# Optimization experiments

Hardware: AMD Instinct MI355X
Metric: run time of the kernel (lower is better)

## Reference

```python
import jax, jax.numpy as jnp
import numpy as np

B, N, L = 2, 2048, 2048
DQ, DKV, H, WF = 1024, 1024, 16, 4
HD = DQ // H
EPS = 1e-5


def _ln(x, g, b):
    m = jnp.mean(x, axis=-1, keepdims=True)
    v = jnp.mean(jnp.square(x - m), axis=-1, keepdims=True)
    return (x - m) * jax.lax.rsqrt(v + EPS) * g + b


def setup_inputs() -> dict:
    key = jax.random.key(0)
    ks = jax.random.split(key, 12)
    s = 0.02
    return {
        "x_q": jax.random.normal(ks[0], (B, N, DQ), jnp.float32),
        "x_kv": jax.random.normal(ks[1], (B, L, DKV), jnp.float32),
        "qn_g": jnp.ones((DQ,), jnp.float32),
        "qn_b": jnp.zeros((DQ,), jnp.float32),
        "kvn_g": jnp.ones((DKV,), jnp.float32),
        "kvn_b": jnp.zeros((DKV,), jnp.float32),
        "Wq": jax.random.normal(ks[2], (DQ, DQ), jnp.float32) * s,
        "bq": jnp.zeros((DQ,), jnp.float32),
        "Wk": jax.random.normal(ks[3], (DQ, DKV), jnp.float32) * s,
        "bk": jnp.zeros((DQ,), jnp.float32),
        "Wv": jax.random.normal(ks[4], (DQ, DKV), jnp.float32) * s,
        "bv": jnp.zeros((DQ,), jnp.float32),
        "Wo": jax.random.normal(ks[5], (DQ, DQ), jnp.float32) * s,
        "bo": jnp.zeros((DQ,), jnp.float32),
        "n2_g": jnp.ones((DQ,), jnp.float32),
        "n2_b": jnp.zeros((DQ,), jnp.float32),
        "W1": jax.random.normal(ks[6], (WF * DQ, DQ), jnp.float32) * s,
        "b1": jnp.zeros((WF * DQ,), jnp.float32),
        "W2": jax.random.normal(ks[7], (DQ, WF * DQ), jnp.float32) * s,
        "b2": jnp.zeros((DQ,), jnp.float32),
    }


def reference(x_q, x_kv, qn_g, qn_b, kvn_g, kvn_b, Wq, bq, Wk, bk, Wv, bv,
              Wo, bo, n2_g, n2_b, W1, b1, W2, b2):
    # projections (torch Linear: x @ W.T + b)
    q = (_ln(x_q, qn_g, qn_b) @ Wq.T + bq).reshape(B, N, H, HD)
    kvn = _ln(x_kv, kvn_g, kvn_b)
    k = (kvn @ Wk.T + bk).reshape(B, L, H, HD)
    v = (kvn @ Wv.T + bv).reshape(B, L, H, HD)

    # attention with softmax-1: exp(s)/(1 + sum exp(s)), numerically stable
    scale = 1.0 / jnp.sqrt(jnp.float32(HD))
    s = jnp.einsum("bnhd,blhd->bhnl", q, k) * scale  # [B,H,N,L]
    m = jnp.max(s, axis=-1, keepdims=True)
    m = jnp.maximum(m, 0.0)  # include the implicit zero logit of softmax-1
    p = jnp.exp(s - m)
    denom = jnp.sum(p, axis=-1, keepdims=True) + jnp.exp(-m)
    attn = p / denom
    attn_out = jnp.einsum("bhnl,blhd->bnhd", attn, v).reshape(B, N, DQ)

    # residual + out proj
    x = x_q + (attn_out @ Wo.T + bo)
    # residual MLP (GELU, exact/erf as torch nn.GELU default)
    h = jax.nn.gelu(_ln(x, n2_g, n2_b) @ W1.T + b1, approximate=False)
    x = x + (h @ W2.T + b2)
    return x
```

## Files before the change

### kernel.cpp

```cpp
#include <hip/hip_runtime.h>
#include <hip/hip_bf16.h>
#include <stdint.h>

#define DEV __device__ __forceinline__

typedef unsigned short ushort_t;
typedef __attribute__((ext_vector_type(8))) short bf16x8;
typedef __attribute__((ext_vector_type(4))) float f32x4;

DEV uint32_t f2bf2(float lo, float hi) {
  uint32_t d;
  asm("v_cvt_pk_bf16_f32 %0, %1, %2" : "=v"(d) : "v"(lo), "v"(hi));
  return d;
}
DEV ushort_t f2bf(float f) { return (ushort_t)f2bf2(f, f); }

DEV void gload_lds16(const void* gp, void* lp) {
  __builtin_amdgcn_global_load_lds(
      (__attribute__((address_space(1))) void*)(void*)(uintptr_t)gp,
      (__attribute__((address_space(3))) void*)lp, 16, 0, 0);
}

__global__ __launch_bounds__(256) void cvt_all(
    const float* __restrict__ Wq, const float* __restrict__ Wk,
    const float* __restrict__ Wv, const float* __restrict__ Wo,
    const float* __restrict__ W1, const float* __restrict__ W2,
    ushort_t* __restrict__ WQKVB, ushort_t* __restrict__ WoB,
    ushort_t* __restrict__ W1B, ushort_t* __restrict__ W2B) {
  int i = blockIdx.x * 256 + threadIdx.x;
  const float* src; ushort_t* dst; int j;
  if (i < 262144)            { src = Wq; dst = WQKVB;            j = i; }
  else if (i < 524288)       { src = Wk; dst = WQKVB + 1048576;  j = i - 262144; }
  else if (i < 786432)       { src = Wv; dst = WQKVB + 2097152;  j = i - 524288; }
  else if (i < 1048576)      { src = Wo; dst = WoB;              j = i - 786432; }
  else if (i < 2097152)      { src = W1; dst = W1B;              j = i - 1048576; }
  else                       { src = W2; dst = W2B;              j = i - 2097152; }
  float4 v = ((const float4*)src)[j];
  uint2 o; o.x = f2bf2(v.x, v.y); o.y = f2bf2(v.z, v.w);
  ((uint2*)dst)[j] = o;
}

DEV void ln_row(const float* __restrict__ x, const float* __restrict__ g,
                const float* __restrict__ be, ushort_t* __restrict__ out, int row) {
  const int t = threadIdx.x;
  const float4 v = ((const float4*)(x + (size_t)row * 1024))[t];
  float s = v.x + v.y + v.z + v.w;
  float sq = v.x * v.x + v.y * v.y + v.z * v.z + v.w * v.w;
#pragma unroll
  for (int d = 1; d < 64; d <<= 1) { s += __shfl_xor(s, d); sq += __shfl_xor(sq, d); }
  __shared__ float sm[8];
  const int w = t >> 6, lane = t & 63;
  if (lane == 0) { sm[w * 2] = s; sm[w * 2 + 1] = sq; }
  __syncthreads();
  s = sm[0] + sm[2] + sm[4] + sm[6];
  sq = sm[1] + sm[3] + sm[5] + sm[7];
  const float mean = s * (1.f / 1024.f);
  const float var = sq * (1.f / 1024.f) - mean * mean;
  const float rstd = rsqrtf(var + 1e-5f);
  const float4 gv = ((const float4*)g)[t];
  const float4 bv = ((const float4*)be)[t];
  uint2 o;
  o.x = f2bf2((v.x - mean) * rstd * gv.x + bv.x, (v.y - mean) * rstd * gv.y + bv.y);
  o.y = f2bf2((v.z - mean) * rstd * gv.z + bv.z, (v.w - mean) * rstd * gv.w + bv.w);
  ((uint2*)(out + (size_t)row * 1024))[t] = o;
}

__global__ __launch_bounds__(256) void ln_bf16(const float* __restrict__ x,
                                               const float* __restrict__ g,
                                               const float* __restrict__ be,
                                               ushort_t* __restrict__ out) {
  ln_row(x, g, be, out, blockIdx.x);
}

__global__ __launch_bounds__(256) void ln_fused(
    const float* __restrict__ x_q, const float* __restrict__ x_kv,
    const float* __restrict__ qg, const float* __restrict__ qb,
    const float* __restrict__ kg, const float* __restrict__ kb,
    ushort_t* __restrict__ oq, ushort_t* __restrict__ okv) {
  const int r = blockIdx.x;
  if (r < 4096) ln_row(x_q, qg, qb, oq, r);
  else ln_row(x_kv, kg, kb, okv, r - 4096);
}

DEV void xcd_remap(int gx, int gy, int& bx, int& by) {
  const int lin = by * gx + bx;
  const int xcd = lin & 7, s = lin >> 3;
  by = xcd * (gy >> 3) + s / gx;
  bx = s % gx;
}

enum { EPI_BF16 = 0, EPI_KV = 1, EPI_RESID = 2, EPI_GELU = 3, EPI_QKV = 4 };

template <int TN, int BK, int EPI>
__global__ __launch_bounds__(256, 3) void gemm_bt(
    const ushort_t* __restrict__ A,
    const ushort_t* __restrict__ A2,
    const ushort_t* __restrict__ Wb,
    const float* __restrict__ bias, const float* __restrict__ bias2,
    const float* __restrict__ bias3,
    const float* __restrict__ resid,
    void* __restrict__ outp, void* __restrict__ outp2, void* __restrict__ outp3,
    int M, int N, int K, float oscale) {
  constexpr int NI = (TN == 128) ? 4 : 2;
  constexpr int CH = BK / 8;
  constexpr int NA = (128 * CH) / 256;
  constexpr int NBL = (TN * CH) / 256;
  constexpr int KS = BK / 32;
  __shared__ ushort_t As[2][128 * BK];
  __shared__ ushort_t Bs[2][TN * BK];
  const int t = threadIdx.x;
  const int w = t >> 6, lane = t & 63;
  const int qd = lane >> 4, ql = lane & 15;
  int bx = blockIdx.x, by = blockIdx.y;
  xcd_remap(gridDim.x, gridDim.y, bx, by);
  const int m0 = by * 128, n0 = bx * TN;
  const int wm = (TN == 128) ? (w >> 1) * 64 : w * 32;
  const int wn = (TN == 128) ? (w & 1) * 64 : 0;
  const int sw = (BK == 64) ? (ql & 7) : ((ql >> 1) & 3);

  const ushort_t* Ause = (EPI == EPI_QKV && n0 >= 1024) ? A2 : A;

  const ushort_t* pa[NA];
#pragma unroll
  for (int p = 0; p < NA; p++) {
    int n = p * 256 + t, row = n / CH, c = n % CH;
    int g = (BK == 64) ? (c ^ (row & 7)) : (c ^ ((row >> 1) & 3));
    pa[p] = Ause + (size_t)(m0 + row) * K + g * 8;
  }
  const ushort_t* pb[NBL];
#pragma unroll
  for (int p = 0; p < NBL; p++) {
    int n = p * 256 + t, row = n / CH, c = n % CH;
    int g = (BK == 64) ? (c ^ (row & 7)) : (c ^ ((row >> 1) & 3));
    pb[p] = Wb + (size_t)(n0 + row) * K + g * 8;
  }

#pragma unroll
  for (int p = 0; p < NA; p++) { gload_lds16(pa[p], &As[0][(p * 256 + t) * 8]); pa[p] += BK; }
#pragma unroll
  for (int p = 0; p < NBL; p++) { gload_lds16(pb[p], &Bs[0][(p * 256 + t) * 8]); pb[p] += BK; }
  __syncthreads();

  f32x4 acc[NI][4] = {};
  const int NIT = K / BK;
  int cur = 0;

  for (int it = 0; it < NIT; ++it) {
    if (it + 1 < NIT) {
#pragma unroll
      for (int p = 0; p < NA; p++) { gload_lds16(pa[p], &As[1 ^ cur][(p * 256 + t) * 8]); pa[p] += BK; }
#pragma unroll
      for (int p = 0; p < NBL; p++) { gload_lds16(pb[p], &Bs[1 ^ cur][(p * 256 + t) * 8]); pb[p] += BK; }
    }
    const ushort_t* Ac = As[cur];
    const ushort_t* Bc = Bs[cur];
#pragma unroll
    for (int ks = 0; ks < KS; ks++) {
      bf16x8 af[NI], bf[4];
#pragma unroll
      for (int i = 0; i < NI; i++)
        af[i] = *(const bf16x8*)&Ac[(wm + i * 16 + ql) * BK + ((ks * 4 + qd) ^ sw) * 8];
#pragma unroll
      for (int j = 0; j < 4; j++)
        bf[j] = *(const bf16x8*)&Bc[(wn + j * 16 + ql) * BK + ((ks * 4 + qd) ^ sw) * 8];
#pragma unroll
      for (int i = 0; i < NI; i++)
#pragma unroll
        for (int j = 0; j < 4; j++)
          acc[i][j] = __builtin_amdgcn_mfma_f32_16x16x32_bf16(af[i], bf[j], acc[i][j], 0, 0, 0);
    }
    __syncthreads();
    cur ^= 1;
  }

#pragma unroll
  for (int i = 0; i < NI; i++) {
    const int mr = m0 + wm + i * 16 + qd * 4;
#pragma unroll
    for (int j = 0; j < 4; j++) {
      const int col = n0 + wn + j * 16 + ql;
      f32x4 v = acc[i][j];
      if constexpr (EPI == EPI_BF16) {
        const float bb = bias[col];
        ushort_t* o = (ushort_t*)outp;
#pragma unroll
        for (int r = 0; r < 4; r++) o[(size_t)(mr + r) * N + col] = f2bf((v[r] + bb) * oscale);
      } else if constexpr (EPI == EPI_QKV) {
        if (col < 1024) {
          const float bb = bias[col];
          ushort_t* o = (ushort_t*)outp;
#pragma unroll
          for (int r = 0; r < 4; r++) o[(size_t)(mr + r) * 1024 + col] = f2bf((v[r] + bb) * oscale);
        } else if (col < 2048) {
          const int c2 = col - 1024;
          const float bb = bias2[c2];
          ushort_t* o = (ushort_t*)outp2;
#pragma unroll
          for (int r = 0; r < 4; r++) o[(size_t)(mr + r) * 1024 + c2] = f2bf(v[r] + bb);
        } else {
          const int vc = col - 2048;
          const float bb = bias3[vc];
          const int h = vc >> 6, d = vc & 63;
          const int b = mr >> 11, l0 = mr & 2047;
          uint2 pk;
          pk.x = f2bf2(v[0] + bb, v[1] + bb);
          pk.y = f2bf2(v[2] + bb, v[3] + bb);
          *(uint2*)((ushort_t*)outp3 + ((((size_t)b * 16 + h) * 64 + d) * 2048 + l0)) = pk;
        }
      } else if constexpr (EPI == EPI_RESID) {
        const float bb = bias[col];
        float* o = (float*)outp;
#pragma unroll
        for (int r = 0; r < 4; r++) {
          size_t idx = (size_t)(mr + r) * N + col;
          o[idx] = resid[idx] + v[r] + bb;
        }
      } else if constexpr (EPI == EPI_GELU) {
        const float bb = bias[col];
        ushort_t* o = (ushort_t*)outp;
#pragma unroll
        for (int r = 0; r < 4; r++) {
          float x = v[r] + bb;
          float gx = 0.5f * x * (1.0f + erff(x * 0.70710678118654752f));
          o[(size_t)(mr + r) * N + col] = f2bf(gx);
        }
      }
    }
  }
}

__global__ __launch_bounds__(256, 2) void flash_attn(const ushort_t* __restrict__ Qg,
                                                     const ushort_t* __restrict__ Kg,
                                                     const ushort_t* __restrict__ VTg,
                                                     ushort_t* __restrict__ Og) {
  __shared__ ushort_t QPs[128 * 64];
  __shared__ ushort_t Ks[2][64 * 64];
  __shared__ ushort_t Vs[2][64 * 64];
  const int t = threadIdx.x, w = t >> 6, lane = t & 63;
  const int qd = lane >> 4, ql = lane & 15;
  int bx = blockIdx.x, bh = blockIdx.y;
  xcd_remap(gridDim.x, gridDim.y, bx, bh);
  const int b = bh >> 4, h = bh & 15;
  const int n0 = bx * 128;
  const ushort_t* Qp = Qg + ((size_t)b * 2048 + n0) * 1024 + h * 64;
  const ushort_t* Kp = Kg + (size_t)b * 2048 * 1024 + h * 64;
  const ushort_t* Vp = VTg + (size_t)bh * 64 * 2048;
  const int sw = ql & 7;

  const ushort_t* kp2[2];
  const ushort_t* vp2[2];
#pragma unroll
  for (int p = 0; p < 2; p++) {
    int n = p * 256 + t, row = n >> 3, c = (n & 7) ^ (row & 7);
    kp2[p] = Kp + (size_t)row * 1024 + c * 8;
    vp2[p] = Vp + (size_t)row * 2048 + c * 8;
  }

#pragma unroll
  for (int p = 0; p < 4; p++) {
    int n = p * 256 + t, row = n >> 3, c = (n & 7) ^ (row & 7);
    gload_lds16(Qp + (size_t)row * 1024 + c * 8, &QPs[n * 8]);
  }
#pragma unroll
  for (int p = 0; p < 2; p++) {
    int n = p * 256 + t;
    gload_lds16(kp2[p], &Ks[0][n * 8]);
    gload_lds16(vp2[p], &Vs[0][n * 8]);
    kp2[p] += 64 * 1024;
    vp2[p] += 64;
  }
  __syncthreads();

  bf16x8 aq[2][2];
#pragma unroll
  for (int i = 0; i < 2; i++)
#pragma unroll
    for (int ks = 0; ks < 2; ks++)
      aq[i][ks] = *(const bf16x8*)&QPs[(w * 32 + i * 16 + ql) * 64 + ((ks * 4 + qd) ^ sw) * 8];
  __syncthreads();

  f32x4 accO[2][4] = {};
  float lro2[2] = {0.f, 0.f};

  int cur = 0;
  for (int lt = 0; lt < 32; ++lt) {
    if (lt + 1 < 32) {
#pragma unroll
      for (int p = 0; p < 2; p++) {
        int n = p * 256 + t;
        gload_lds16(kp2[p], &Ks[1 ^ cur][n * 8]);
        gload_lds16(vp2[p], &Vs[1 ^ cur][n * 8]);
        kp2[p] += 64 * 1024;
        vp2[p] += 64;
      }
    }
    const ushort_t* Kc = Ks[cur];
    const ushort_t* Vc = Vs[cur];

    f32x4 accS[4][2] = {};
#pragma unroll
    for (int ks = 0; ks < 2; ks++) {
      bf16x8 bk[4];
#pragma unroll
      for (int j = 0; j < 4; j++)
        bk[j] = *(const bf16x8*)&Kc[(j * 16 + ql) * 64 + ((ks * 4 + qd) ^ sw) * 8];
#pragma unroll
      for (int j = 0; j < 4; j++)
#pragma unroll
        for (int i = 0; i < 2; i++)
          accS[j][i] = __builtin_amdgcn_mfma_f32_16x16x32_bf16(bk[j], aq[i][ks], accS[j][i], 0, 0, 0);
    }

#pragma unroll
    for (int j = 0; j < 4; j++)
#pragma unroll
      for (int i = 0; i < 2; i++) {
        f32x4 p;
#pragma unroll
        for (int r = 0; r < 4; r++) {
          p[r] = __builtin_amdgcn_exp2f(accS[j][i][r]);
          lro2[i] += p[r];
        }
        const int n = w * 32 + i * 16 + ql;
        const int coff = (((j * 2 + (qd >> 1)) ^ sw) << 3) + ((qd & 1) << 2);
        uint2 pk; pk.x = f2bf2(p[0], p[1]); pk.y = f2bf2(p[2], p[3]);
        *(uint2*)&QPs[n * 64 + coff] = pk;
      }

#pragma unroll
    for (int ks = 0; ks < 2; ks++) {
      bf16x8 ap[2], bv[4];
#pragma unroll
      for (int i = 0; i < 2; i++)
        ap[i] = *(const bf16x8*)&QPs[(w * 32 + i * 16 + ql) * 64 + ((ks * 4 + qd) ^ sw) * 8];
#pragma unroll
      for (int jo = 0; jo < 4; jo++)
        bv[jo] = *(const bf16x8*)&Vc[(jo * 16 + ql) * 64 + ((ks * 4 + qd) ^ sw) * 8];
#pragma unroll
      for (int i = 0; i < 2; i++)
#pragma unroll
        for (int jo = 0; jo < 4; jo++)
          accO[i][jo] = __builtin_amdgcn_mfma_f32_16x16x32_bf16(ap[i], bv[jo], accO[i][jo], 0, 0, 0);
    }

    __syncthreads();
    cur ^= 1;
  }

  float dn[2];
#pragma unroll
  for (int i = 0; i < 2; i++) {
    float l = lro2[i];
    l += __shfl_xor(l, 16);
    l += __shfl_xor(l, 32);
    dn[i] = l + 1.0f;
  }

#pragma unroll
  for (int i = 0; i < 2; i++)
#pragma unroll
    for (int r = 0; r < 4; r++) {
      const float inv = 1.0f / __shfl(dn[i], qd * 4 + r);
      const int row = n0 + w * 32 + i * 16 + qd * 4 + r;
#pragma unroll
      for (int jo = 0; jo < 4; jo++)
        Og[((size_t)b * 2048 + row) * 1024 + h * 64 + jo * 16 + ql] =
            f2bf(accO[i][jo][r] * inv);
    }
}

extern "C" void kernel_launch(void* const* d_in, const int* in_sizes, int n_in,
                              void* d_out, int out_size, void* d_ws, size_t ws_size,
                              hipStream_t stream) {
  const float* x_q = (const float*)d_in[0];
  const float* x_kv = (const float*)d_in[1];
  const float* qn_g = (const float*)d_in[2];
  const float* qn_b = (const float*)d_in[3];
  const float* kvn_g = (const float*)d_in[4];
  const float* kvn_b = (const float*)d_in[5];
  const float* Wq = (const float*)d_in[6];
  const float* bq = (const float*)d_in[7];
  const float* Wk = (const float*)d_in[8];
  const float* bk = (const float*)d_in[9];
  const float* Wv = (const float*)d_in[10];
  const float* bv = (const float*)d_in[11];
  const float* Wo = (const float*)d_in[12];
  const float* bo = (const float*)d_in[13];
  const float* n2_g = (const float*)d_in[14];
  const float* n2_b = (const float*)d_in[15];
  const float* W1 = (const float*)d_in[16];
  const float* b1 = (const float*)d_in[17];
  const float* W2 = (const float*)d_in[18];
  const float* b2 = (const float*)d_in[19];

  char* ws = (char*)d_ws;
  const size_t MB = 1ull << 20;
  ushort_t* WQKVB = (ushort_t*)(ws + 0 * MB);
  ushort_t* WoB = (ushort_t*)(ws + 6 * MB);
  ushort_t* W1B = (ushort_t*)(ws + 8 * MB);
  ushort_t* W2B = (ushort_t*)(ws + 16 * MB);
  ushort_t* LNQ = (ushort_t*)(ws + 24 * MB);
  ushort_t* LNKV = (ushort_t*)(ws + 32 * MB);
  ushort_t* Qb = (ushort_t*)(ws + 40 * MB);
  ushort_t* Kb = (ushort_t*)(ws + 48 * MB);
  ushort_t* VTb = (ushort_t*)(ws + 56 * MB);
  ushort_t* AOb = (ushort_t*)(ws + 64 * MB);
  float* Xf = (float*)(ws + 72 * MB);
  ushort_t* LN2 = (ushort_t*)(ws + 88 * MB);
  ushort_t* Hb = (ushort_t*)(ws + 24 * MB);

  const float QSCALE = 0.18033688011112042f;

  cvt_all<<<12288, 256, 0, stream>>>(Wq, Wk, Wv, Wo, W1, W2, WQKVB, WoB, W1B, W2B);
  ln_fused<<<8192, 256, 0, stream>>>(x_q, x_kv, qn_g, qn_b, kvn_g, kvn_b, LNQ, LNKV);

  gemm_bt<128, 32, EPI_QKV><<<dim3(24, 32), 256, 0, stream>>>(
      LNQ, LNKV, WQKVB, bq, bk, bv, nullptr, Qb, Kb, VTb, 4096, 3072, 1024, QSCALE);

  flash_attn<<<dim3(16, 32), 256, 0, stream>>>(Qb, Kb, VTb, AOb);

  gemm_bt<64, 64, EPI_RESID><<<dim3(16, 32), 256, 0, stream>>>(
      AOb, nullptr, WoB, bo, nullptr, nullptr, x_q, Xf, nullptr, nullptr,
      4096, 1024, 1024, 1.0f);
  ln_bf16<<<4096, 256, 0, stream>>>(Xf, n2_g, n2_b, LN2);
  gemm_bt<128, 32, EPI_GELU><<<dim3(32, 32), 256, 0, stream>>>(
      LN2, nullptr, W1B, b1, nullptr, nullptr, nullptr, Hb, nullptr, nullptr,
      4096, 4096, 1024, 1.0f);
  gemm_bt<64, 64, EPI_RESID><<<dim3(16, 32), 256, 0, stream>>>(
      Hb, nullptr, W2B, b2, nullptr, nullptr, Xf, (float*)d_out, nullptr, nullptr,
      4096, 1024, 4096, 1.0f);
}
```

Baseline: 366.3 us.

## Split-K the Wo and W2 GEMMs with atomic accumulation into residual buffers

The two N=1024 output GEMMs now run as split-K with two K-slices each, accumulating via float atomic adds. The residual is seeded by copying x_q into Xf during the first layernorm and Xf into the output during the second layernorm. This doubles the block count of the narrow GEMMs to raise occupancy and drops the separate residual read from their epilogue. In exchange it adds atomic traffic, an extra fp32 copy in the layernorm kernels, and a summation order that is no longer deterministic.

```diff
diff --git a/kernel.cpp b/kernel.cpp
--- a/kernel.cpp
+++ b/kernel.cpp
@@ -19,6 +19,15 @@
   __builtin_amdgcn_global_load_lds(
       (__attribute__((address_space(1))) void*)(void*)(uintptr_t)gp,
       (__attribute__((address_space(3))) void*)lp, 16, 0, 0);
+}
+
+DEV void gfadd(float* p, float v) {
+#if __has_builtin(__builtin_amdgcn_global_atomic_fadd_f32)
+  __builtin_amdgcn_global_atomic_fadd_f32(
+      (__attribute__((address_space(1))) float*)(void*)(uintptr_t)p, v);
+#else
+  atomicAdd(p, v);
+#endif
 }
 
 __global__ __launch_bounds__(256) void cvt_all(
@@ -41,9 +50,11 @@
 }
 
 DEV void ln_row(const float* __restrict__ x, const float* __restrict__ g,
-                const float* __restrict__ be, ushort_t* __restrict__ out, int row) {
+                const float* __restrict__ be, ushort_t* __restrict__ out, int row,
+                float* __restrict__ cpy) {
   const int t = threadIdx.x;
   const float4 v = ((const float4*)(x + (size_t)row * 1024))[t];
+  if (cpy) ((float4*)(cpy + (size_t)row * 1024))[t] = v;
   float s = v.x + v.y + v.z + v.w;
   float sq = v.x * v.x + v.y * v.y + v.z * v.z + v.w * v.w;
 #pragma unroll
@@ -68,18 +79,20 @@
 __global__ __launch_bounds__(256) void ln_bf16(const float* __restrict__ x,
                                                const float* __restrict__ g,
                                                const float* __restrict__ be,
-                                               ushort_t* __restrict__ out) {
-  ln_row(x, g, be, out, blockIdx.x);
+                                               ushort_t* __restrict__ out,
+                                               float* __restrict__ cpy) {
+  ln_row(x, g, be, out, blockIdx.x, cpy);
 }
 
 __global__ __launch_bounds__(256) void ln_fused(
     const float* __restrict__ x_q, const float* __restrict__ x_kv,
     const float* __restrict__ qg, const float* __restrict__ qb,
     const float* __restrict__ kg, const float* __restrict__ kb,
-    ushort_t* __restrict__ oq, ushort_t* __restrict__ okv) {
+    ushort_t* __restrict__ oq, ushort_t* __restrict__ okv,
+    float* __restrict__ cpyq) {
   const int r = blockIdx.x;
-  if (r < 4096) ln_row(x_q, qg, qb, oq, r);
-  else ln_row(x_kv, kg, kb, okv, r - 4096);
+  if (r < 4096) ln_row(x_q, qg, qb, oq, r, cpyq);
+  else ln_row(x_kv, kg, kb, okv, r - 4096, nullptr);
 }
 
 DEV void xcd_remap(int gx, int gy, int& bx, int& by) {
@@ -89,7 +102,7 @@
   bx = s % gx;
 }
 
-enum { EPI_BF16 = 0, EPI_KV = 1, EPI_RESID = 2, EPI_GELU = 3, EPI_QKV = 4 };
+enum { EPI_BF16 = 0, EPI_KV = 1, EPI_RESID = 2, EPI_GELU = 3, EPI_QKV = 4, EPI_ATOMIC = 5 };
 
 template <int TN, int BK, int EPI>
 __global__ __launch_bounds__(256, 3) void gemm_bt(
@@ -100,7 +113,7 @@
     const float* __restrict__ bias3,
     const float* __restrict__ resid,
     void* __restrict__ outp, void* __restrict__ outp2, void* __restrict__ outp3,
-    int M, int N, int K, float oscale) {
+    int M, int N, int K, int Kstride, float oscale) {
   constexpr int NI = (TN == 128) ? 4 : 2;
   constexpr int CH = BK / 8;
   constexpr int NA = (128 * CH) / 256;
@@ -112,6 +125,7 @@
   const int w = t >> 6, lane = t & 63;
   const int qd = lane >> 4, ql = lane & 15;
   int bx = blockIdx.x, by = blockIdx.y;
+  const int kz = blockIdx.z;
   xcd_remap(gridDim.x, gridDim.y, bx, by);
   const int m0 = by * 128, n0 = bx * TN;
   const int wm = (TN == 128) ? (w >> 1) * 64 : w * 32;
@@ -119,20 +133,21 @@
   const int sw = (BK == 64) ? (ql & 7) : ((ql >> 1) & 3);
 
   const ushort_t* Ause = (EPI == EPI_QKV && n0 >= 1024) ? A2 : A;
+  const size_t k0 = (size_t)kz * K;
 
   const ushort_t* pa[NA];
 #pragma unroll
   for (int p = 0; p < NA; p++) {
     int n = p * 256 + t, row = n / CH, c = n % CH;
     int g = (BK == 64) ? (c ^ (row & 7)) : (c ^ ((row >> 1) & 3));
-    pa[p] = Ause + (size_t)(m0 + row) * K + g * 8;
+    pa[p] = Ause + (size_t)(m0 + row) * Kstride + k0 + g * 8;
   }
   const ushort_t* pb[NBL];
 #pragma unroll
   for (int p = 0; p < NBL; p++) {
     int n = p * 256 + t, row = n / CH, c = n % CH;
     int g = (BK == 64) ? (c ^ (row & 7)) : (c ^ ((row >> 1) & 3));
-    pb[p] = Wb + (size_t)(n0 + row) * K + g * 8;
+    pb[p] = Wb + (size_t)(n0 + row) * Kstride + k0 + g * 8;
   }
 
 #pragma unroll
@@ -215,6 +230,11 @@
           size_t idx = (size_t)(mr + r) * N + col;
           o[idx] = resid[idx] + v[r] + bb;
         }
+      } else if constexpr (EPI == EPI_ATOMIC) {
+        const float bb = (kz == 0) ? bias[col] : 0.f;
+        float* o = (float*)outp;
+#pragma unroll
+        for (int r = 0; r < 4; r++) gfadd(&o[(size_t)(mr + r) * N + col], v[r] + bb);
       } else if constexpr (EPI == EPI_GELU) {
         const float bb = bias[col];
         ushort_t* o = (ushort_t*)outp;
@@ -412,21 +432,21 @@
   const float QSCALE = 0.18033688011112042f;
 
   cvt_all<<<12288, 256, 0, stream>>>(Wq, Wk, Wv, Wo, W1, W2, WQKVB, WoB, W1B, W2B);
-  ln_fused<<<8192, 256, 0, stream>>>(x_q, x_kv, qn_g, qn_b, kvn_g, kvn_b, LNQ, LNKV);
+  ln_fused<<<8192, 256, 0, stream>>>(x_q, x_kv, qn_g, qn_b, kvn_g, kvn_b, LNQ, LNKV, Xf);
 
   gemm_bt<128, 32, EPI_QKV><<<dim3(24, 32), 256, 0, stream>>>(
-      LNQ, LNKV, WQKVB, bq, bk, bv, nullptr, Qb, Kb, VTb, 4096, 3072, 1024, QSCALE);
+      LNQ, LNKV, WQKVB, bq, bk, bv, nullptr, Qb, Kb, VTb, 4096, 3072, 1024, 1024, QSCALE);
 
   flash_attn<<<dim3(16, 32), 256, 0, stream>>>(Qb, Kb, VTb, AOb);
 
-  gemm_bt<64, 64, EPI_RESID><<<dim3(16, 32), 256, 0, stream>>>(
-      AOb, nullptr, WoB, bo, nullptr, nullptr, x_q, Xf, nullptr, nullptr,
-      4096, 1024, 1024, 1.0f);
-  ln_bf16<<<4096, 256, 0, stream>>>(Xf, n2_g, n2_b, LN2);
+  gemm_bt<64, 64, EPI_ATOMIC><<<dim3(16, 32, 2), 256, 0, stream>>>(
+      AOb, nullptr, WoB, bo, nullptr, nullptr, nullptr, Xf, nullptr, nullptr,
+      4096, 1024, 512, 1024, 1.0f);
+  ln_bf16<<<4096, 256, 0, stream>>>(Xf, n2_g, n2_b, LN2, (float*)d_out);
   gemm_bt<128, 32, EPI_GELU><<<dim3(32, 32), 256, 0, stream>>>(
       LN2, nullptr, W1B, b1, nullptr, nullptr, nullptr, Hb, nullptr, nullptr,
-      4096, 4096, 1024, 1.0f);
-  gemm_bt<64, 64, EPI_RESID><<<dim3(16, 32), 256, 0, stream>>>(
-      Hb, nullptr, W2B, b2, nullptr, nullptr, Xf, (float*)d_out, nullptr, nullptr,
-      4096, 1024, 4096, 1.0f);
-}
+      4096, 4096, 1024, 1024, 1.0f);
+  gemm_bt<64, 64, EPI_ATOMIC><<<dim3(16, 32, 2), 256, 0, stream>>>(
+      Hb, nullptr, W2B, b2, nullptr, nullptr, nullptr, (float*)d_out, nullptr, nullptr,
+      4096, 1024, 2048, 4096, 1.0f);
+}
```

Measured after the change: 408.6 us. 11.5% more time.
